# Kernel tuning notes

Measured on AMD Instinct MI355X. Metric: run time of the kernel, lower is better.

## Reference

```python
import jax, jax.numpy as jnp
import numpy as np

NEG_SLOPE = 0.2
EPS = 1e-16

N_NODES = 50000
N_EDGES = 800000
IN_CH = 128
HEADS = 4
OUT_CH = 32


def setup_inputs() -> dict:
    key = jax.random.key(0)
    k1, k2, k3, k4, k5 = jax.random.split(key, 5)
    x = jax.random.normal(k1, (N_NODES, IN_CH), dtype=jnp.float32)
    edge_index = jax.random.randint(k2, (2, N_EDGES), 0, N_NODES, dtype=jnp.int64)
    # Glorot-ish scaling for stability
    W = jax.random.normal(k3, (IN_CH, HEADS * OUT_CH), dtype=jnp.float32) / np.sqrt(IN_CH)
    att_src = jax.random.normal(k4, (HEADS, OUT_CH), dtype=jnp.float32) / np.sqrt(OUT_CH)
    att_dst = jax.random.normal(k5, (HEADS, OUT_CH), dtype=jnp.float32) / np.sqrt(OUT_CH)
    bias = jnp.zeros((HEADS * OUT_CH,), dtype=jnp.float32)
    return {"x": x, "edge_index": edge_index, "W": W,
            "att_src": att_src, "att_dst": att_dst, "bias": bias}


def reference(x, edge_index, W, att_src, att_dst, bias):
    N = x.shape[0]
    H, C = att_src.shape

    # PyG GATConv default: add self-loops
    self_loop = jnp.arange(N, dtype=edge_index.dtype)
    src = jnp.concatenate([edge_index[0], self_loop])  # [E+N]
    dst = jnp.concatenate([edge_index[1], self_loop])  # [E+N]

    # Linear transform, split heads: [N, H, C]
    h = (x @ W).reshape(N, H, C)

    # Per-node attention logits: [N, H]
    a_src = jnp.sum(h * att_src[None], axis=-1)
    a_dst = jnp.sum(h * att_dst[None], axis=-1)

    # Per-edge logits with LeakyReLU: [E+N, H]
    e = a_src[src] + a_dst[dst]
    e = jnp.where(e >= 0, e, NEG_SLOPE * e)

    # Segment softmax over destination-node neighborhoods
    e_max = jax.ops.segment_max(e, dst, num_segments=N)  # [N, H]
    e_exp = jnp.exp(e - e_max[dst])
    denom = jax.ops.segment_sum(e_exp, dst, num_segments=N)  # [N, H]
    alpha = e_exp / (denom[dst] + EPS)  # [E+N, H]

    # Weighted scatter-aggregate of messages: [N, H, C]
    msgs = h[src] * alpha[:, :, None]
    out = jax.ops.segment_sum(msgs, dst, num_segments=N)

    out = out.reshape(N, H * C) + bias  # concat heads + bias
    return jax.nn.relu(out)  # wrapper activation (dropout=0 is identity)
```

## Files before the change

kernel.cpp:

```cpp
#include <hip/hip_runtime.h>
#include <hip/hip_bf16.h>
#include <math.h>

#define NEG_SLOPE 0.2f
#define EPS_F 1e-16f
#define PCAP 4096
#define NPMAX 512

typedef float f32x4 __attribute__((ext_vector_type(4)));
typedef short bf16x8 __attribute__((ext_vector_type(8)));

__device__ __forceinline__ unsigned int pk2bf(float a, float b) {
    unsigned int ua = __float_as_uint(a), ub = __float_as_uint(b);
    ua = (ua + 0x7fffu + ((ua >> 16) & 1u)) >> 16;
    ub = (ub + 0x7fffu + ((ub >> 16) & 1u)) >> 16;
    return ua | (ub << 16);
}
__device__ __forceinline__ unsigned short f2bf(float f) {
    unsigned int u = __float_as_uint(f);
    return (unsigned short)((u + 0x7fffu + ((u >> 16) & 1u)) >> 16);
}
__device__ __forceinline__ float bf_lo(unsigned int p) { return __uint_as_float(p << 16); }
__device__ __forceinline__ float bf_hi(unsigned int p) { return __uint_as_float(p & 0xffff0000u); }

__global__ __launch_bounds__(256)
void k_front(const unsigned int* __restrict__ eidx,
             int* __restrict__ pcnt, unsigned int* __restrict__ rec, int E, int npart,
             const float* __restrict__ W,
             const float* __restrict__ att_src, const float* __restrict__ att_dst,
             unsigned short* __restrict__ Wtb, int nPB) {
    __shared__ int hist[NPMAX];
    __shared__ int base[NPMAX];
    __shared__ int sflag;
    int t = threadIdx.x;

    if ((int)blockIdx.x < nPB) {
        if (t < 64) {
            unsigned int v = eidx[2 * t + 1];
            #pragma unroll
            for (int m = 1; m <= 32; m <<= 1) v |= __shfl_xor(v, m);
            if (t == 0) sflag = (v == 0u) ? 1 : 0;
        }
        for (int p = t; p < npart; p += 256) hist[p] = 0;
        __syncthreads();
        int flag = sflag;
        int e0 = blockIdx.x * 4096;
        int se[16], de[16];
        #pragma unroll
        for (int i = 0; i < 16; i++) {
            int idx = e0 + t + i * 256;
            de[i] = -1;
            if (idx < E) {
                if (flag) { se[i] = (int)eidx[2 * idx]; de[i] = (int)eidx[2 * (E + idx)]; }
                else      { se[i] = (int)eidx[idx];     de[i] = (int)eidx[E + idx]; }
                atomicAdd(&hist[de[i] >> 7], 1);
            }
        }
        __syncthreads();
        for (int p = t; p < npart; p += 256) {
            int c = hist[p];
            base[p] = c ? atomicAdd(&pcnt[p], c) : 0;
            hist[p] = 0;
        }
        __syncthreads();
        #pragma unroll
        for (int i = 0; i < 16; i++) {
            if (de[i] >= 0) {
                int p = de[i] >> 7;
                int r = atomicAdd(&hist[p], 1);
                int pos = base[p] + r;
                if (pos < PCAP)
                    rec[(size_t)p * PCAP + pos] =
                        ((unsigned int)se[i] << 7) | (unsigned int)(de[i] & 127);
            }
        }
    } else {
        int b = (int)blockIdx.x - nPB;
        if (b < 64) {
            int id = b * 256 + t;
            int k = id >> 7, col = id & 127;
            Wtb[col * 128 + k] = f2bf(W[id]);
        } else {
            int k4 = t >> 3, j = t & 7;
            const float* att = (j < 4) ? att_src : att_dst;
            int h = j & 3;
            #pragma unroll
            for (int kk = 0; kk < 4; kk++) {
                int k = k4 * 4 + kk;
                float s = 0.f;
                #pragma unroll
                for (int c = 0; c < 32; c++)
                    s = fmaf(W[k * 128 + h * 32 + c], att[h * 32 + c], s);
                Wtb[(128 + j) * 128 + k] = f2bf(s);
            }
            for (int idx = t; idx < 1024; idx += 256)
                Wtb[(136 + (idx >> 7)) * 128 + (idx & 127)] = 0;
        }
    }
}

__global__ __launch_bounds__(256)
void k_mid(const float* __restrict__ x, const unsigned short* __restrict__ Wtb,
           unsigned short* __restrict__ hb,
           float* __restrict__ a_src, float* __restrict__ a_dst, int N,
           const int* __restrict__ pcnt, const unsigned int* __restrict__ rec,
           unsigned int* __restrict__ srt, int* __restrict__ rowArr,
           int* __restrict__ degArr, int gb) {
    __shared__ __align__(16) char smem[53248];
    int t = threadIdx.x;

    if ((int)blockIdx.x < gb) {
        unsigned short* xlds = (unsigned short*)smem;
        unsigned short* wlds = (unsigned short*)(smem + 16384);
        int l = t & 63, w = t >> 6;
        int br = blockIdx.x * 64;

        #pragma unroll
        for (int i = 0; i < 9; i++) {
            int u = t + i * 256;
            uint4 v = *(const uint4*)(Wtb + u * 8);
            int row = u >> 4;
            int e8  = (u & 15) * 8;
            *(uint4*)&wlds[row * 128 + (e8 ^ ((row & 7) << 3))] = v;
        }
        {
            int row = t >> 2, kq = t & 3;
            int gr = br + row;
            const float* xp = x + (size_t)gr * 128 + kq * 32;
            #pragma unroll
            for (int j = 0; j < 4; j++) {
                uint4 pk = make_uint4(0u, 0u, 0u, 0u);
                if (gr < N) {
                    float4 v0 = *(const float4*)(xp + j * 8);
                    float4 v1 = *(const float4*)(xp + j * 8 + 4);
                    pk.x = pk2bf(v0.x, v0.y); pk.y = pk2bf(v0.z, v0.w);
                    pk.z = pk2bf(v1.x, v1.y); pk.w = pk2bf(v1.z, v1.w);
                }
                int e8 = kq * 32 + j * 8;
                *(uint4*)&xlds[row * 128 + (e8 ^ ((row & 7) << 3))] = pk;
            }
        }
        __syncthreads();

        bf16x8 a[4];
        int arow = w * 16 + (l & 15);
        int ae   = (l >> 4) * 8;
        #pragma unroll
        for (int kc = 0; kc < 4; kc++)
            a[kc] = *(const bf16x8*)&xlds[arow * 128 + ((kc * 32 + ae) ^ ((arow & 7) << 3))];

        int rowbase = br + w * 16 + (l >> 4) * 4;

        #pragma unroll
        for (int nb = 0; nb < 9; nb++) {
            int brow = nb * 16 + (l & 15);
            f32x4 c = {0.f, 0.f, 0.f, 0.f};
            #pragma unroll
            for (int kc = 0; kc < 4; kc++) {
                bf16x8 bfr = *(const bf16x8*)&wlds[brow * 128 + ((kc * 32 + ae) ^ ((brow & 7) << 3))];
                c = __builtin_amdgcn_mfma_f32_16x16x32_bf16(a[kc], bfr, c, 0, 0, 0);
            }
            if (nb < 8) {
                #pragma unroll
                for (int r = 0; r < 4; r++) {
                    float v  = c[r];
                    float vo = __shfl_xor(v, 1);
                    int row = rowbase + r;
                    if (row < N && (l & 1) == 0)
                        *(unsigned int*)&hb[(size_t)row * 128 + nb * 16 + (l & 15)] = pk2bf(v, vo);
                }
            } else {
                int j = l & 15;
                #pragma unroll
                for (int r = 0; r < 4; r++) {
                    int row = rowbase + r;
                    if (row < N && j < 8) {
                        if (j < 4) a_src[row * 4 + j]     = c[r];
                        else       a_dst[row * 4 + j - 4] = c[r];
                    }
                }
            }
        }
    } else {
        int* hist = (int*)smem;
        int* offs = hist + 128;
        int* cur  = offs + 128;
        unsigned int* ssort = (unsigned int*)(smem + 1536);
        int p = (int)blockIdx.x - gb;
        if (t < 128) { hist[t] = 0; cur[t] = 0; }
        __syncthreads();
        int cnt = min(pcnt[p], PCAP);
        const unsigned int* rb = rec + (size_t)p * PCAP;
        for (int i = t; i < cnt; i += 256) atomicAdd(&hist[rb[i] & 127], 1);
        __syncthreads();
        if (t < 128) offs[t] = hist[t];
        __syncthreads();
        #pragma unroll
        for (int off = 1; off < 128; off <<= 1) {
            int u = (t < 128 && t >= off) ? offs[t - off] : 0;
            __syncthreads();
            if (t < 128) offs[t] += u;
            __syncthreads();
        }
        for (int i = t; i < cnt; i += 256) {
            unsigned int r = rb[i];
            int n = r & 127;
            int pos = (offs[n] - hist[n]) + atomicAdd(&cur[n], 1);
            ssort[pos] = r >> 7;
        }
        __syncthreads();
        for (int i = t; i < cnt; i += 256) srt[(size_t)p * PCAP + i] = ssort[i];
        int node = (p << 7) + t;
        if (t < 128 && node < N) {
            rowArr[node] = p * PCAP + (offs[t] - hist[t]);
            degArr[node] = hist[t];
        }
    }
}

__global__ __launch_bounds__(256)
void k_aggregate(const unsigned int* __restrict__ srt, const int* __restrict__ rowArr,
                 const int* __restrict__ degArr,
                 const float* __restrict__ a_src, const float* __restrict__ a_dst,
                 const unsigned short* __restrict__ hb,
                 const float* __restrict__ bias,
                 float* __restrict__ out, int N) {
    int wave = threadIdx.x >> 6;
    int lane = threadIdx.x & 63;
    int d = blockIdx.x * 4 + wave;
    if (d >= N) return;
    int c0 = lane * 2;
    int head = lane >> 4;

    float ad = a_dst[d * 4 + head];

    float es = a_src[d * 4 + head] + ad;
    es = fmaxf(es, NEG_SLOPE * es);
    float wself = __expf(es);
    unsigned int hp = *(const unsigned int*)&hb[(size_t)d * 128 + c0];
    float accx = wself * bf_lo(hp);
    float accy = wself * bf_hi(hp);
    float den  = wself;

    const unsigned int* bk = srt + rowArr[d];
    int g = degArr[d];
    int j = 0;
    for (; j + 7 < g; j += 8) {
        int s[8]; float as[8]; unsigned int p[8];
        #pragma unroll
        for (int q = 0; q < 8; q++) s[q] = (int)bk[j + q];
        #pragma unroll
        for (int q = 0; q < 8; q++) as[q] = a_src[s[q] * 4 + head];
        #pragma unroll
        for (int q = 0; q < 8; q++) p[q] = *(const unsigned int*)&hb[(size_t)s[q] * 128 + c0];
        #pragma unroll
        for (int q = 0; q < 8; q++) {
            float ev = as[q] + ad;
            ev = fmaxf(ev, NEG_SLOPE * ev);
            float w0 = __expf(ev);
            den += w0;
            accx = fmaf(w0, bf_lo(p[q]), accx);
            accy = fmaf(w0, bf_hi(p[q]), accy);
        }
    }
    for (; j < g; j++) {
        int s0 = (int)bk[j];
        float as0 = a_src[s0 * 4 + head];
        unsigned int p0 = *(const unsigned int*)&hb[(size_t)s0 * 128 + c0];
        float ev = as0 + ad;
        ev = fmaxf(ev, NEG_SLOPE * ev);
        float w0 = __expf(ev);
        den += w0;
        accx = fmaf(w0, bf_lo(p0), accx);
        accy = fmaf(w0, bf_hi(p0), accy);
    }

    float rden = 1.f / (den + EPS_F);
    float2 b2 = *(const float2*)&bias[c0];
    float ox = fmaxf(accx * rden + b2.x, 0.f);
    float oy = fmaxf(accy * rden + b2.y, 0.f);
    *(float2*)&out[(size_t)d * 128 + c0] = make_float2(ox, oy);
}

extern "C" void kernel_launch(void* const* d_in, const int* in_sizes, int n_in,
                              void* d_out, int out_size, void* d_ws, size_t ws_size,
                              hipStream_t stream) {
    const float* x        = (const float*)d_in[0];
    const unsigned int* e = (const unsigned int*)d_in[1];
    const float* W        = (const float*)d_in[2];
    const float* att_src  = (const float*)d_in[3];
    const float* att_dst  = (const float*)d_in[4];
    const float* bias     = (const float*)d_in[5];
    float* out            = (float*)d_out;

    int N = in_sizes[0] / 128;
    int E = in_sizes[1] / 2;
    int npart = (N + 127) >> 7;

    char* ws = (char*)d_ws;
    size_t off = 0;
    unsigned short* Wtb    = (unsigned short*)(ws + off); off += 144 * 128 * 2;
    unsigned short* hb     = (unsigned short*)(ws + off); off += (size_t)N * 128 * 2;
    float*          a_src  = (float*)(ws + off);          off += (size_t)N * 16;
    float*          a_dst  = (float*)(ws + off);          off += (size_t)N * 16;
    int*            rowArr = (int*)(ws + off);            off += (size_t)N * 4;
    int*            degArr = (int*)(ws + off);            off += (size_t)N * 4;
    int*            pcnt   = (int*)(ws + off);            off += (size_t)NPMAX * 4;
    unsigned int*   rec    = (unsigned int*)(ws + off);   off += (size_t)npart * PCAP * 4;
    unsigned int*   srt    = (unsigned int*)(ws + off);   off += (size_t)npart * PCAP * 4;

    int nPB = (E + 4095) / 4096;
    int gb  = (N + 63) / 64;

    hipMemsetAsync(pcnt, 0, (size_t)NPMAX * 4, stream);

    k_front<<<nPB + 65, 256, 0, stream>>>(e, pcnt, rec, E, npart,
                                          W, att_src, att_dst, Wtb, nPB);
    k_mid<<<gb + npart, 256, 0, stream>>>(x, Wtb, hb, a_src, a_dst, N,
                                          pcnt, rec, srt, rowArr, degArr, gb);
    k_aggregate<<<(N + 3) / 4, 256, 0, stream>>>(srt, rowArr, degArr,
                                                 a_src, a_dst, hb, bias, out, N);
}
```

Before: 85.85 us.

## Split aggregation wave into two half-waves over edges with 8-byte gathers

The aggregation kernel now has each half of a wave handle alternate neighbor edges. Each lane loads four bf16 channels (8 bytes) instead of two, and the halves are combined with a cross-lane shuffle at the end. The attention projection is pre-scaled by log2(e) so exp2f replaces __expf, removing a multiply per edge. Edge-index loads for the 64-bit path use uint2 reads. Together these aim for more memory-level parallelism per wave and wider gathers, at the cost of a final shuffle reduction and a half-idle store.

```diff
diff --git a/kernel.cpp b/kernel.cpp
--- a/kernel.cpp
+++ b/kernel.cpp
@@ -6,6 +6,7 @@
 #define EPS_F 1e-16f
 #define PCAP 4096
 #define NPMAX 512
+#define LOG2E 1.44269504088896f
 
 typedef float f32x4 __attribute__((ext_vector_type(4)));
 typedef short bf16x8 __attribute__((ext_vector_type(8)));
@@ -44,6 +45,7 @@
         for (int p = t; p < npart; p += 256) hist[p] = 0;
         __syncthreads();
         int flag = sflag;
+        const uint2* e2p = (const uint2*)eidx;
         int e0 = blockIdx.x * 4096;
         int se[16], de[16];
         #pragma unroll
@@ -51,8 +53,8 @@
             int idx = e0 + t + i * 256;
             de[i] = -1;
             if (idx < E) {
-                if (flag) { se[i] = (int)eidx[2 * idx]; de[i] = (int)eidx[2 * (E + idx)]; }
-                else      { se[i] = (int)eidx[idx];     de[i] = (int)eidx[E + idx]; }
+                if (flag) { se[i] = (int)e2p[idx].x; de[i] = (int)e2p[E + idx].x; }
+                else      { se[i] = (int)eidx[idx];  de[i] = (int)eidx[E + idx]; }
                 atomicAdd(&hist[de[i] >> 7], 1);
             }
         }
@@ -91,7 +93,7 @@
                 #pragma unroll
                 for (int c = 0; c < 32; c++)
                     s = fmaf(W[k * 128 + h * 32 + c], att[h * 32 + c], s);
-                Wtb[(128 + j) * 128 + k] = f2bf(s);
+                Wtb[(128 + j) * 128 + k] = f2bf(s * LOG2E);
             }
             for (int idx = t; idx < 1024; idx += 256)
                 Wtb[(136 + (idx >> 7)) * 128 + (idx & 127)] = 0;
@@ -227,59 +229,86 @@
                  float* __restrict__ out, int N) {
     int wave = threadIdx.x >> 6;
     int lane = threadIdx.x & 63;
+    int half = lane >> 5;
+    int li   = lane & 31;
+    int c4   = li * 4;
+    int head = li >> 3;
     int d = blockIdx.x * 4 + wave;
     if (d >= N) return;
-    int c0 = lane * 2;
-    int head = lane >> 4;
 
     float ad = a_dst[d * 4 + head];
 
-    float es = a_src[d * 4 + head] + ad;
-    es = fmaxf(es, NEG_SLOPE * es);
-    float wself = __expf(es);
-    unsigned int hp = *(const unsigned int*)&hb[(size_t)d * 128 + c0];
-    float accx = wself * bf_lo(hp);
-    float accy = wself * bf_hi(hp);
-    float den  = wself;
+    float den = 0.f, a0 = 0.f, a1 = 0.f, a2 = 0.f, a3 = 0.f;
+    if (half == 0) {
+        float es = a_src[d * 4 + head] + ad;
+        es = fmaxf(es, NEG_SLOPE * es);
+        float w = exp2f(es);
+        uint2 hv = *(const uint2*)&hb[(size_t)d * 128 + c4];
+        den = w;
+        a0 = w * bf_lo(hv.x); a1 = w * bf_hi(hv.x);
+        a2 = w * bf_lo(hv.y); a3 = w * bf_hi(hv.y);
+    }
 
     const unsigned int* bk = srt + rowArr[d];
     int g = degArr[d];
     int j = 0;
-    for (; j + 7 < g; j += 8) {
-        int s[8]; float as[8]; unsigned int p[8];
-        #pragma unroll
-        for (int q = 0; q < 8; q++) s[q] = (int)bk[j + q];
-        #pragma unroll
-        for (int q = 0; q < 8; q++) as[q] = a_src[s[q] * 4 + head];
-        #pragma unroll
-        for (int q = 0; q < 8; q++) p[q] = *(const unsigned int*)&hb[(size_t)s[q] * 128 + c0];
-        #pragma unroll
-        for (int q = 0; q < 8; q++) {
-            float ev = as[q] + ad;
-            ev = fmaxf(ev, NEG_SLOPE * ev);
-            float w0 = __expf(ev);
-            den += w0;
-            accx = fmaf(w0, bf_lo(p[q]), accx);
-            accy = fmaf(w0, bf_hi(p[q]), accy);
-        }
-    }
-    for (; j < g; j++) {
-        int s0 = (int)bk[j];
-        float as0 = a_src[s0 * 4 + head];
-        unsigned int p0 = *(const unsigned int*)&hb[(size_t)s0 * 128 + c0];
-        float ev = as0 + ad;
-        ev = fmaxf(ev, NEG_SLOPE * ev);
-        float w0 = __expf(ev);
+    for (; j + 8 <= g; j += 8) {
+        int s0 = (int)bk[j + 0 + half];
+        int s1 = (int)bk[j + 2 + half];
+        int s2 = (int)bk[j + 4 + half];
+        int s3 = (int)bk[j + 6 + half];
+        float e0 = a_src[s0 * 4 + head];
+        float e1 = a_src[s1 * 4 + head];
+        float e2 = a_src[s2 * 4 + head];
+        float e3 = a_src[s3 * 4 + head];
+        uint2 p0 = *(const uint2*)&hb[(size_t)s0 * 128 + c4];
+        uint2 p1 = *(const uint2*)&hb[(size_t)s1 * 128 + c4];
+        uint2 p2 = *(const uint2*)&hb[(size_t)s2 * 128 + c4];
+        uint2 p3 = *(const uint2*)&hb[(size_t)s3 * 128 + c4];
+        e0 += ad; e0 = fmaxf(e0, NEG_SLOPE * e0);
+        e1 += ad; e1 = fmaxf(e1, NEG_SLOPE * e1);
+        e2 += ad; e2 = fmaxf(e2, NEG_SLOPE * e2);
+        e3 += ad; e3 = fmaxf(e3, NEG_SLOPE * e3);
+        float w0 = exp2f(e0), w1 = exp2f(e1), w2 = exp2f(e2), w3 = exp2f(e3);
+        den += (w0 + w1) + (w2 + w3);
+        a0 = fmaf(w0, bf_lo(p0.x), a0); a1 = fmaf(w0, bf_hi(p0.x), a1);
+        a2 = fmaf(w0, bf_lo(p0.y), a2); a3 = fmaf(w0, bf_hi(p0.y), a3);
+        a0 = fmaf(w1, bf_lo(p1.x), a0); a1 = fmaf(w1, bf_hi(p1.x), a1);
+        a2 = fmaf(w1, bf_lo(p1.y), a2); a3 = fmaf(w1, bf_hi(p1.y), a3);
+        a0 = fmaf(w2, bf_lo(p2.x), a0); a1 = fmaf(w2, bf_hi(p2.x), a1);
+        a2 = fmaf(w2, bf_lo(p2.y), a2); a3 = fmaf(w2, bf_hi(p2.y), a3);
+        a0 = fmaf(w3, bf_lo(p3.x), a0); a1 = fmaf(w3, bf_hi(p3.x), a1);
+        a2 = fmaf(w3, bf_lo(p3.y), a2); a3 = fmaf(w3, bf_hi(p3.y), a3);
+    }
+    for (; j < g; j += 2) {
+        int idx = j + half;
+        bool val = idx < g;
+        int s0 = (int)bk[val ? idx : (g - 1)];
+        float e0 = a_src[s0 * 4 + head] + ad;
+        e0 = fmaxf(e0, NEG_SLOPE * e0);
+        float w0 = val ? exp2f(e0) : 0.f;
+        uint2 p0 = *(const uint2*)&hb[(size_t)s0 * 128 + c4];
         den += w0;
-        accx = fmaf(w0, bf_lo(p0), accx);
-        accy = fmaf(w0, bf_hi(p0), accy);
-    }
-
-    float rden = 1.f / (den + EPS_F);
-    float2 b2 = *(const float2*)&bias[c0];
-    float ox = fmaxf(accx * rden + b2.x, 0.f);
-    float oy = fmaxf(accy * rden + b2.y, 0.f);
-    *(float2*)&out[(size_t)d * 128 + c0] = make_float2(ox, oy);
+        a0 = fmaf(w0, bf_lo(p0.x), a0); a1 = fmaf(w0, bf_hi(p0.x), a1);
+        a2 = fmaf(w0, bf_lo(p0.y), a2); a3 = fmaf(w0, bf_hi(p0.y), a3);
+    }
+
+    den += __shfl_xor(den, 32);
+    a0  += __shfl_xor(a0, 32);
+    a1  += __shfl_xor(a1, 32);
+    a2  += __shfl_xor(a2, 32);
+    a3  += __shfl_xor(a3, 32);
+
+    if (half == 0) {
+        float rden = 1.f / (den + EPS_F);
+        float4 b4 = *(const float4*)&bias[c4];
+        float4 o;
+        o.x = fmaxf(a0 * rden + b4.x, 0.f);
+        o.y = fmaxf(a1 * rden + b4.y, 0.f);
+        o.z = fmaxf(a2 * rden + b4.z, 0.f);
+        o.w = fmaxf(a3 * rden + b4.w, 0.f);
+        *(float4*)&out[(size_t)d * 128 + c4] = o;
+    }
 }
 
 extern "C" void kernel_launch(void* const* d_in, const int* in_sizes, int n_in,
```

After: 84.90 us. Within noise of the previous version (-1.1%).
